# Performance work log

Hardware: AMD Instinct MI355X
Metric: run time of the kernel (lower is better)

Reference implementation:

```python
import jax, jax.numpy as jnp
import numpy as np

B, S, H, R, F, E, K = 4, 2048, 1024, 256, 4096, 8, 2


def setup_inputs() -> dict:
    key = jax.random.key(0)
    k = jax.random.split(key, 7)
    s = 0.02
    return {
        "x": jax.random.normal(k[0], (B, S, H), dtype=jnp.float32),
        "router_w": jax.random.normal(k[1], (H, E), dtype=jnp.float32) * s,
        "router_b": jnp.zeros((E,), dtype=jnp.float32),
        "w1": jax.random.normal(k[2], (E, H, R), dtype=jnp.float32) * s,  # expert Linear(hidden->rank), no bias
        "w2": jax.random.normal(k[3], (E, R, F), dtype=jnp.float32) * s,  # expert Linear(rank->ffn), no bias
        "lin2_w": jax.random.normal(k[4], (F, H), dtype=jnp.float32) * s,
        "lin2_b": jnp.zeros((H,), dtype=jnp.float32),
    }


def reference(x, router_w, router_b, w1, w2, lin2_w, lin2_b):
    # Router: softmax over experts, top-k selection (mask), weight by softmax prob
    logits = jnp.einsum("bsh,he->bse", x, router_w) + router_b
    routing_weights = jax.nn.softmax(logits, axis=-1)            # [B,S,E]
    _, topk_idx = jax.lax.top_k(routing_weights, K)              # [B,S,K]
    mask = jnp.sum(jax.nn.one_hot(topk_idx, E, dtype=x.dtype), axis=-2)  # [B,S,E] in {0,1}
    mw = routing_weights * mask                                  # mask * weight per expert

    # Dense per-expert low-rank FFN (original computes all experts, masks after).
    # Fold mask*weight into the rank-space activations to avoid a [B,S,E,F] tensor.
    t = jnp.einsum("bsh,ehr->bser", x, w1)                       # [B,S,E,R]
    t = t * mw[..., None]
    mixed = jnp.einsum("bser,erf->bsf", t, w2)                   # [B,S,F]

    h = jax.nn.gelu(mixed, approximate=False)                    # torch nn.GELU is erf-based
    out = jnp.einsum("bsf,fh->bsh", h, lin2_w) + lin2_b
    # dropout is identity in eval mode
    return out
```

## Files before the change

### kernel.cpp

```cpp
#include <hip/hip_runtime.h>
#include <math.h>


using short8  = __attribute__((ext_vector_type(8))) short;
using floatx4 = __attribute__((ext_vector_type(4))) float;
typedef unsigned short bf16_t;

#define TOK   8192
#define HDIM  1024
#define RDIM  256
#define FDIM  4096
#define NEXP  8
#define MAXTILES 96
#define MAXSLOTS 16384
#define IMG   16384

__device__ __forceinline__ bf16_t f2bf(float f) {
  union { float f; unsigned u; } a; a.f = f;
  unsigned u = a.u;
  return (bf16_t)((u + 0x7FFFu + ((u >> 16) & 1u)) >> 16);
}

__device__ __forceinline__ float gelu_erf(float v) {
  return 0.5f * v * (1.0f + erff(v * 0.70710678118654752f));
}

__device__ __forceinline__ void gload16(const void* g, void* l) {
  __builtin_amdgcn_global_load_lds(
      (const __attribute__((address_space(1))) void*)g,
      (__attribute__((address_space(3))) void*)l, 16, 0, 0);
}

__device__ __forceinline__ int swz_off(int r, int kl) {
  return r * 128 + ((((kl >> 3) ^ (r & 15)) << 3) | (kl & 7));
}


__device__ __forceinline__ void pack_tile_body(const float* __restrict__ src,
                                               size_t kStride,
                                               bf16_t* __restrict__ img,
                                               bf16_t* __restrict__ lim) {
  const int tid = threadIdx.x;
  const int rr = tid & 127, half = tid >> 7;
  for (int kl = half; kl < 128; kl += 2)
    lim[swz_off(rr, kl)] = f2bf(src[(size_t)kl * kStride + rr]);
  __syncthreads();
  const int4* s4 = (const int4*)lim;
  int4* d4 = (int4*)img;
#pragma unroll
  for (int i = 0; i < 8; i++) d4[tid + i * 256] = s4[tid + i * 256];
}

__global__ __launch_bounds__(256)
void prep(const float* __restrict__ x, const float* __restrict__ rw,
          const float* __restrict__ rb, const float* __restrict__ w1,
          const float* __restrict__ w2, const float* __restrict__ l2w,
          int* __restrict__ gid_tok, float2* __restrict__ tokscale,
          bf16_t* __restrict__ xb, bf16_t* __restrict__ w1p,
          bf16_t* __restrict__ w2p, bf16_t* __restrict__ ltw,
          int* __restrict__ tokslot, float2* __restrict__ slotsc) {
  __shared__ __align__(16) char smem[33280];
  const int b = blockIdx.x;
  const int t = threadIdx.x;

  if (b < 2048) {
    const int token = b * 4 + (t >> 6);
    const int lane  = t & 63;
    const float* xr = x + (size_t)token * HDIM;
    bf16_t* xbr = xb + (size_t)token * HDIM;
    double acc[NEXP];
#pragma unroll
    for (int e = 0; e < NEXP; e++) acc[e] = 0.0;
    for (int h = lane; h < HDIM; h += 64) {
      const float xf = xr[h];
      xbr[h] = f2bf(xf);
      const double xv = (double)xf;
      const float* wr = rw + (size_t)h * NEXP;
#pragma unroll
      for (int e = 0; e < NEXP; e++) acc[e] += xv * (double)wr[e];
    }
#pragma unroll
    for (int off = 32; off > 0; off >>= 1) {
#pragma unroll
      for (int e = 0; e < NEXP; e++) acc[e] += __shfl_xor(acc[e], off, 64);
    }
    double lg[NEXP];
#pragma unroll
    for (int e = 0; e < NEXP; e++) lg[e] = acc[e] + (double)rb[e];
    double mx = lg[0];
#pragma unroll
    for (int e = 1; e < NEXP; e++) mx = fmax(mx, lg[e]);
    double p[NEXP]; double den = 0.0;
#pragma unroll
    for (int e = 0; e < NEXP; e++) { p[e] = exp(lg[e] - mx); den += p[e]; }
    int i1 = 0;
#pragma unroll
    for (int e = 1; e < NEXP; e++) if (lg[e] > lg[i1]) i1 = e;
    int i2 = (i1 == 0) ? 1 : 0;
#pragma unroll
    for (int e = 0; e < NEXP; e++)
      if (e != i1 && e != i2 && lg[e] > lg[i2]) i2 = e;
    if (lane == 0) {
      const int elo = min(i1, i2), ehi = max(i1, i2);
      gid_tok[token] = elo * 8 + ehi;
      tokscale[token] = make_float2((float)(p[elo] / den), (float)(p[ehi] / den));
    }
  } else if (b < 2176) {
    const int img = b - 2048;
    const int e = img >> 4, nc = (img >> 3) & 1, kb = img & 7;
    pack_tile_body(w1 + (size_t)e * 1024 * 256 + (size_t)kb * 128 * 256 + nc * 128,
                   256, w1p + (size_t)img * IMG, (bf16_t*)smem);
  } else if (b < 2688) {
    const int img = b - 2176;
    const int n = img >> 4, e = (img >> 1) & 7, kb = img & 1;
    pack_tile_body(w2 + (size_t)e * 256 * 4096 + (size_t)kb * 128 * 4096 + n * 128,
                   4096, w2p + (size_t)img * IMG, (bf16_t*)smem);
  } else if (b < 3712) {
    float* tile = (float*)smem;
    const int bid = b - 2688;
    const int c0 = (bid & 15) * 64;
    const int r0 = (bid >> 4) * 64;
    const int tx = t & 63, ty = t >> 6;
#pragma unroll
    for (int i = 0; i < 64; i += 4)
      tile[(ty + i) * 65 + tx] = l2w[(size_t)(r0 + ty + i) * HDIM + (c0 + tx)];
    __syncthreads();
#pragma unroll
    for (int i = 0; i < 64; i += 4)
      ltw[(size_t)(c0 + ty + i) * FDIM + (r0 + tx)] = f2bf(tile[tx * 65 + ty + i]);
  } else {
    const int i = (b - 3712) * 256 + t;
    tokslot[i] = -1;
    slotsc[i] = make_float2(0.f, 0.f);
  }
}


__global__ void build_scatter(const int* __restrict__ gid_tok,
                              const float2* __restrict__ tokscale,
                              int* __restrict__ ctrl,
                              int* __restrict__ tok_of_slot,
                              float2* __restrict__ scale_of_slot) {
  __shared__ int hist[64], ntl[64], start[64], fill[64];
  const int t = threadIdx.x;
  if (t < 64) { hist[t] = 0; fill[t] = 0; }
  __syncthreads();
  for (int i = t; i < TOK; i += 256) atomicAdd(&hist[gid_tok[i]], 1);
  __syncthreads();
  if (t < 64) ntl[t] = (hist[t] + 127) >> 7;
  __syncthreads();
  if (t < 64) {
    int slot0 = 0, tile0 = 0;
    for (int g = 0; g < t; g++) { slot0 += ntl[g] << 7; tile0 += ntl[g]; }
    start[t] = slot0;
    const int nt = ntl[t], c = hist[t];
    for (int i = 0; i < nt; i++) {
      ctrl[256 + (tile0 + i) * 3 + 0] = t;
      ctrl[256 + (tile0 + i) * 3 + 1] = slot0 + i * 128;
      ctrl[256 + (tile0 + i) * 3 + 2] = min(128, c - i * 128);
    }
    if (t == 63) ctrl[192] = tile0 + nt;
  }
  __syncthreads();
  for (int i = t; i < TOK; i += 256) {
    const int g = gid_tok[i];
    const int pos = atomicAdd(&fill[g], 1);
    const int slot = start[g] + pos;
    tok_of_slot[slot] = i;
    scale_of_slot[slot] = tokscale[i];
  }
}

__global__ __launch_bounds__(256)
void gemm_g1(const bf16_t* __restrict__ xb, const bf16_t* __restrict__ w1p,
             bf16_t* __restrict__ Tp, const int* __restrict__ ctrl,
             const int* __restrict__ tok_of_slot,
             const float2* __restrict__ scale_of_slot) {
  const int b = blockIdx.x;
  const int n = b & 3, mh = (b >> 2) & 1, tile = b >> 3;
  if (tile >= ctrl[192]) return;
  const int nrows = ctrl[256 + tile * 3 + 2];
  if (mh && nrows <= 64) return;
  __shared__ bf16_t As[64 * 128];
  __shared__ bf16_t Bs[128 * 128];
  const int gid   = ctrl[256 + tile * 3];
  const int slot0 = ctrl[256 + tile * 3 + 1];
  const int e = (n < 2) ? (gid >> 3) : (gid & 7);
  const int nc = n & 1;
  const int tid = threadIdx.x, lane = tid & 63, w = tid >> 6;
  const int wm = (w & 1) * 32, wn = (w >> 1) * 64;
  const int l16 = lane & 15, quad = lane >> 4;

  floatx4 acc[2][4];
  const floatx4 zero = {0.f, 0.f, 0.f, 0.f};
#pragma unroll
  for (int i = 0; i < 2; i++)
#pragma unroll
    for (int j = 0; j < 4; j++) acc[i][j] = zero;

  int toks[4];
  int rowAs[4];
#pragma unroll
  for (int i = 0; i < 4; i++) {
    rowAs[i] = w * 16 + i * 4 + (lane >> 4);
    int tk = tok_of_slot[slot0 + mh * 64 + rowAs[i]];
    toks[i] = (tk < 0) ? 0 : tk;
  }
  const bf16_t* bimg = w1p + (size_t)(e * 16 + nc * 8) * IMG;
  bf16_t* lA = As + w * 2048;
  bf16_t* lB = Bs + w * 4096;

  for (int kb = 0; kb < 8; kb++) {
    __syncthreads();
#pragma unroll
    for (int i = 0; i < 4; i++) {
      const int gq = (lane & 15) ^ (rowAs[i] & 15);
      gload16(xb + (size_t)toks[i] * HDIM + kb * 128 + gq * 8, lA + i * 512);
    }
#pragma unroll
    for (int i = 0; i < 8; i++)
      gload16(bimg + (size_t)kb * IMG + w * 4096 + i * 512 + lane * 8, lB + i * 512);
    __syncthreads();
#pragma unroll
    for (int s = 0; s < 4; s++) {
      const int pg = ((s * 4 + quad) ^ l16) << 3;
      short8 af[2], bfr[4];
#pragma unroll
      for (int i = 0; i < 2; i++)
        af[i] = *(const short8*)&As[(wm + i * 16 + l16) * 128 + pg];
#pragma unroll
      for (int i = 0; i < 4; i++)
        bfr[i] = *(const short8*)&Bs[(wn + i * 16 + l16) * 128 + pg];
#pragma unroll
      for (int mi = 0; mi < 2; mi++)
#pragma unroll
        for (int ni = 0; ni < 4; ni++)
          acc[mi][ni] = __builtin_amdgcn_mfma_f32_16x16x32_bf16(
              af[mi], bfr[ni], acc[mi][ni], 0, 0, 0);
    }
  }

  __syncthreads();
#pragma unroll
  for (int mi = 0; mi < 2; mi++) {
#pragma unroll
    for (int r = 0; r < 4; r++) {
      const int rloc = wm + mi * 16 + quad * 4 + r;
      const float2 sc = scale_of_slot[slot0 + mh * 64 + rloc];
      const float s = (n < 2) ? sc.x : sc.y;
#pragma unroll
      for (int ni = 0; ni < 4; ni++) {
        const int c = wn + ni * 16 + l16;
        As[swz_off(rloc, c)] = f2bf(acc[mi][ni][r] * s);
      }
    }
  }
  __syncthreads();
  bf16_t* img = Tp + (size_t)(tile * 4 + n) * IMG + mh * 64 * 128;
  const int4* s4 = (const int4*)As;
  int4* d4 = (int4*)img;
#pragma unroll
  for (int j = 0; j < 4; j++) d4[tid + j * 256] = s4[tid + j * 256];
}

__global__ __launch_bounds__(256)
void gemm_g2(const bf16_t* __restrict__ Tp, const bf16_t* __restrict__ w2p,
             bf16_t* __restrict__ Hb, const int* __restrict__ ctrl,
             const int* __restrict__ tok_of_slot) {
  const int b = blockIdx.x;
  const int n = (b & 7) * 4 + ((b >> 3) & 3);
  const int mh = (b >> 5) & 1, tile = b >> 6;
  if (tile >= ctrl[192]) return;
  const int nrows = ctrl[256 + tile * 3 + 2];
  if (mh && nrows <= 64) return;
  __shared__ bf16_t As[64 * 128];
  __shared__ bf16_t Bs[128 * 128];
  const int gid   = ctrl[256 + tile * 3];
  const int slot0 = ctrl[256 + tile * 3 + 1];
  const int elo = gid >> 3, ehi = gid & 7;
  const int tid = threadIdx.x, lane = tid & 63, w = tid >> 6;
  const int wm = (w & 1) * 32, wn = (w >> 1) * 64;
  const int l16 = lane & 15, quad = lane >> 4;

  floatx4 acc[2][4];
  const floatx4 zero = {0.f, 0.f, 0.f, 0.f};
#pragma unroll
  for (int i = 0; i < 2; i++)
#pragma unroll
    for (int j = 0; j < 4; j++) acc[i][j] = zero;

  const bf16_t* aimg = Tp + (size_t)tile * 4 * IMG + mh * 64 * 128;
  bf16_t* lA = As + w * 2048;
  bf16_t* lB = Bs + w * 4096;

#pragma unroll
  for (int t = 0; t < 4; t++) {
    const int e = (t < 2) ? elo : ehi;
    const bf16_t* bimg = w2p + (size_t)(n * 16 + e * 2 + (t & 1)) * IMG;
    __syncthreads();
#pragma unroll
    for (int i = 0; i < 4; i++)
      gload16(aimg + (size_t)t * IMG + w * 2048 + i * 512 + lane * 8, lA + i * 512);
#pragma unroll
    for (int i = 0; i < 8; i++)
      gload16(bimg + w * 4096 + i * 512 + lane * 8, lB + i * 512);
    __syncthreads();
#pragma unroll
    for (int s = 0; s < 4; s++) {
      const int pg = ((s * 4 + quad) ^ l16) << 3;
      short8 af[2], bfr[4];
#pragma unroll
      for (int i = 0; i < 2; i++)
        af[i] = *(const short8*)&As[(wm + i * 16 + l16) * 128 + pg];
#pragma unroll
      for (int i = 0; i < 4; i++)
        bfr[i] = *(const short8*)&Bs[(wn + i * 16 + l16) * 128 + pg];
#pragma unroll
      for (int mi = 0; mi < 2; mi++)
#pragma unroll
        for (int ni = 0; ni < 4; ni++)
          acc[mi][ni] = __builtin_amdgcn_mfma_f32_16x16x32_bf16(
              af[mi], bfr[ni], acc[mi][ni], 0, 0, 0);
    }
  }

  __syncthreads();
#pragma unroll
  for (int mi = 0; mi < 2; mi++) {
#pragma unroll
    for (int r = 0; r < 4; r++) {
      const int rloc = wm + mi * 16 + quad * 4 + r;
#pragma unroll
      for (int ni = 0; ni < 4; ni++) {
        const int c = wn + ni * 16 + l16;
        Bs[rloc * 128 + c] = f2bf(gelu_erf(acc[mi][ni][r]));
      }
    }
  }
  __syncthreads();
  const int4* s4 = (const int4*)Bs;
#pragma unroll
  for (int j = 0; j < 4; j++) {
    const int chunk = tid + j * 256;
    const int row = chunk >> 4, off = chunk & 15;
    const int tok = tok_of_slot[slot0 + mh * 64 + row];
    if (tok >= 0)
      *(int4*)(Hb + (size_t)tok * FDIM + n * 128 + off * 8) = s4[chunk];
  }
}

__global__ __launch_bounds__(256)
void gemm_g3(const bf16_t* __restrict__ Hb, const bf16_t* __restrict__ ltw,
             float* __restrict__ out, float* __restrict__ p0) {
  __shared__ bf16_t As[128 * 64];
  __shared__ bf16_t Bs[128 * 64];
  const int b = blockIdx.x;
  const int r0 = b >> 3;
  const int m0 = ((b & 7) * 8 + (r0 & 7)) * 128;
  const int n0 = ((r0 >> 3) & 7) * 128;
  const int kb = r0 >> 6;
  const int tid = threadIdx.x, lane = tid & 63, w = tid >> 6;
  const int wm = (w >> 1) * 64, wn = (w & 1) * 64;
  const int l16 = lane & 15, quad = lane >> 4;
  const int rl = lane >> 3, gg = lane & 7;
  const int gf = (gg ^ rl) * 8;

  floatx4 acc[4][4];
  const floatx4 zero = {0.f, 0.f, 0.f, 0.f};
#pragma unroll
  for (int i = 0; i < 4; i++)
#pragma unroll
    for (int j = 0; j < 4; j++) acc[i][j] = zero;

  const bf16_t* ga[4];
  const bf16_t* gb[4];
#pragma unroll
  for (int c = 0; c < 4; c++) {
    ga[c] = Hb  + (size_t)(m0 + w * 32 + c * 8 + rl) * FDIM + kb * 2048 + gf;
    gb[c] = ltw + (size_t)(n0 + w * 32 + c * 8 + rl) * FDIM + kb * 2048 + gf;
  }
  bf16_t* lA = &As[w * 32 * 64];
  bf16_t* lB = &Bs[w * 32 * 64];

  for (int k0 = 0; k0 < 2048; k0 += 64) {
    __syncthreads();
#pragma unroll
    for (int c = 0; c < 4; c++) { gload16(ga[c], lA + c * 512); ga[c] += 64; }
#pragma unroll
    for (int c = 0; c < 4; c++) { gload16(gb[c], lB + c * 512); gb[c] += 64; }
    __syncthreads();
#pragma unroll
    for (int s = 0; s < 2; s++) {
      const int pg = ((s * 4 + quad) ^ (l16 & 7)) * 8;
      short8 af[4], bfr[4];
#pragma unroll
      for (int i = 0; i < 4; i++)
        af[i] = *(const short8*)&As[(wm + i * 16 + l16) * 64 + pg];
#pragma unroll
      for (int i = 0; i < 4; i++)
        bfr[i] = *(const short8*)&Bs[(wn + i * 16 + l16) * 64 + pg];
#pragma unroll
      for (int mi = 0; mi < 4; mi++)
#pragma unroll
        for (int ni = 0; ni < 4; ni++)
          acc[mi][ni] = __builtin_amdgcn_mfma_f32_16x16x32_bf16(
              af[mi], bfr[ni], acc[mi][ni], 0, 0, 0);
    }
  }

  float* dst = kb ? out : p0;
#pragma unroll
  for (int mi = 0; mi < 4; mi++) {
#pragma unroll
    for (int ni = 0; ni < 4; ni++) {
      const int row = m0 + wm + mi * 16 + quad * 4;
      const int col = n0 + wn + ni * 16 + l16;
#pragma unroll
      for (int r = 0; r < 4; r++)
        dst[(size_t)(row + r) * HDIM + col] = acc[mi][ni][r];
    }
  }
}

__global__ void reduce_out(float* __restrict__ out, const float* __restrict__ p0,
                           const float* __restrict__ bias) {
  const int i4 = blockIdx.x * 256 + threadIdx.x;
  float4 a = ((const float4*)out)[i4];
  float4 p = ((const float4*)p0)[i4];
  float4 bb = ((const float4*)bias)[i4 & 255];
  a.x += p.x + bb.x;
  a.y += p.y + bb.y;
  a.z += p.z + bb.z;
  a.w += p.w + bb.w;
  ((float4*)out)[i4] = a;
}


extern "C" void kernel_launch(void* const* d_in, const int* in_sizes, int n_in,
                              void* d_out, int out_size, void* d_ws, size_t ws_size,
                              hipStream_t stream) {
  const float* x   = (const float*)d_in[0];
  const float* rw  = (const float*)d_in[1];
  const float* rb  = (const float*)d_in[2];
  const float* w1  = (const float*)d_in[3];
  const float* w2  = (const float*)d_in[4];
  const float* l2w = (const float*)d_in[5];
  const float* l2b = (const float*)d_in[6];

  char* ws = (char*)d_ws;
  int*    ctrl     = (int*)   (ws + 0);
  int*    gid_tok  = (int*)   (ws + 4096);
  float2* tokscale = (float2*)(ws + 36864);
  int*    tokslot  = (int*)   (ws + 102400);
  float2* slotsc   = (float2*)(ws + 167936);
  bf16_t* xb  = (bf16_t*)(ws + 1048576);
  bf16_t* w1p = (bf16_t*)(ws + 17825792);
  bf16_t* w2p = (bf16_t*)(ws + 22020096);
  bf16_t* ltw = (bf16_t*)(ws + 38797312);
  bf16_t* Tp  = (bf16_t*)(ws + 47185920);
  bf16_t* Hb  = (bf16_t*)(ws + 59768832);
  float*  p0  = (float*) (ws + 1048576);

  prep<<<3776, 256, 0, stream>>>(x, rw, rb, w1, w2, l2w,
                                 gid_tok, tokscale, xb, w1p, w2p, ltw,
                                 tokslot, slotsc);
  build_scatter<<<1, 256, 0, stream>>>(gid_tok, tokscale, ctrl, tokslot, slotsc);

  gemm_g1<<<8 * MAXTILES, 256, 0, stream>>>(xb, w1p, Tp, ctrl, tokslot, slotsc);
  gemm_g2<<<64 * MAXTILES, 256, 0, stream>>>(Tp, w2p, Hb, ctrl, tokslot);
  gemm_g3<<<1024, 256, 0, stream>>>(Hb, ltw, (float*)d_out, p0);
  reduce_out<<<TOK * HDIM / 1024, 256, 0, stream>>>((float*)d_out, p0, l2b);
}
```

Before: 361.6 us.

## Fuse all stages into one cooperative persistent kernel with grid syncs

Replaces six separate launches with one cooperative kernel that runs the prep, build, scatter and three GEMM phases in grid-strided loops, separated by grid-wide barriers. The final GEMM no longer splits K in two, so the partial-sum buffer and the reduce kernel go away, and the bias is added in the epilogue. The scatter stage is spread across all blocks using global atomics instead of running in a single block. The aim is to remove launch gaps and the extra reduction pass, at the cost of grid-sync overhead, a capped persistent grid of at most 512 blocks that may hurt load balance, and fewer blocks in the last GEMM.

```diff
diff --git a/kernel.cpp b/kernel.cpp
--- a/kernel.cpp
+++ b/kernel.cpp
@@ -1,5 +1,8 @@
 #include <hip/hip_runtime.h>
+#include <hip/hip_cooperative_groups.h>
 #include <math.h>
+
+namespace cg = cooperative_groups;
 
 
 using short8  = __attribute__((ext_vector_type(8))) short;
@@ -12,8 +15,11 @@
 #define FDIM  4096
 #define NEXP  8
 #define MAXTILES 96
-#define MAXSLOTS 16384
 #define IMG   16384
+#define NPREP 3776
+#define NG1   (8 * MAXTILES)
+#define NG2   (64 * MAXTILES)
+#define NG3   512
 
 __device__ __forceinline__ bf16_t f2bf(float f) {
   union { float f; unsigned u; } a; a.f = f;
@@ -36,36 +42,19 @@
 }
 
 
-__device__ __forceinline__ void pack_tile_body(const float* __restrict__ src,
-                                               size_t kStride,
-                                               bf16_t* __restrict__ img,
-                                               bf16_t* __restrict__ lim) {
-  const int tid = threadIdx.x;
-  const int rr = tid & 127, half = tid >> 7;
-  for (int kl = half; kl < 128; kl += 2)
-    lim[swz_off(rr, kl)] = f2bf(src[(size_t)kl * kStride + rr]);
-  __syncthreads();
-  const int4* s4 = (const int4*)lim;
-  int4* d4 = (int4*)img;
-#pragma unroll
-  for (int i = 0; i < 8; i++) d4[tid + i * 256] = s4[tid + i * 256];
-}
-
-__global__ __launch_bounds__(256)
-void prep(const float* __restrict__ x, const float* __restrict__ rw,
-          const float* __restrict__ rb, const float* __restrict__ w1,
-          const float* __restrict__ w2, const float* __restrict__ l2w,
-          int* __restrict__ gid_tok, float2* __restrict__ tokscale,
-          bf16_t* __restrict__ xb, bf16_t* __restrict__ w1p,
-          bf16_t* __restrict__ w2p, bf16_t* __restrict__ ltw,
-          int* __restrict__ tokslot, float2* __restrict__ slotsc) {
-  __shared__ __align__(16) char smem[33280];
-  const int b = blockIdx.x;
+__device__ void phase_prep(int vb, char* smem,
+                           const float* __restrict__ x, const float* __restrict__ rw,
+                           const float* __restrict__ rb, const float* __restrict__ w1,
+                           const float* __restrict__ w2, const float* __restrict__ l2w,
+                           int* __restrict__ gid_tok, float2* __restrict__ tokscale,
+                           bf16_t* __restrict__ xb, bf16_t* __restrict__ w1p,
+                           bf16_t* __restrict__ w2p, bf16_t* __restrict__ ltw,
+                           int* __restrict__ tokslot, float2* __restrict__ slotsc,
+                           int* __restrict__ ctrl) {
   const int t = threadIdx.x;
-
-  if (b < 2048) {
-    const int token = b * 4 + (t >> 6);
-    const int lane  = t & 63;
+  const int lane = t & 63;
+  if (vb < 2048) {
+    const int token = vb * 4 + (t >> 6);
     const float* xr = x + (size_t)token * HDIM;
     bf16_t* xbr = xb + (size_t)token * HDIM;
     double acc[NEXP];
@@ -105,19 +94,31 @@
       gid_tok[token] = elo * 8 + ehi;
       tokscale[token] = make_float2((float)(p[elo] / den), (float)(p[ehi] / den));
     }
-  } else if (b < 2176) {
-    const int img = b - 2048;
-    const int e = img >> 4, nc = (img >> 3) & 1, kb = img & 7;
-    pack_tile_body(w1 + (size_t)e * 1024 * 256 + (size_t)kb * 128 * 256 + nc * 128,
-                   256, w1p + (size_t)img * IMG, (bf16_t*)smem);
-  } else if (b < 2688) {
-    const int img = b - 2176;
-    const int n = img >> 4, e = (img >> 1) & 7, kb = img & 1;
-    pack_tile_body(w2 + (size_t)e * 256 * 4096 + (size_t)kb * 128 * 4096 + n * 128,
-                   4096, w2p + (size_t)img * IMG, (bf16_t*)smem);
-  } else if (b < 3712) {
+  } else if (vb < 2688) {
+    const float* src; bf16_t* dst; size_t ks;
+    if (vb < 2176) {
+      const int img = vb - 2048;
+      const int e = img >> 4, nc = (img >> 3) & 1, kb = img & 7;
+      src = w1 + (size_t)e * 1024 * 256 + (size_t)kb * 128 * 256 + nc * 128;
+      ks = 256; dst = w1p + (size_t)img * IMG;
+    } else {
+      const int img = vb - 2176;
+      const int n = img >> 4, e = (img >> 1) & 7, kb = img & 1;
+      src = w2 + (size_t)e * 256 * 4096 + (size_t)kb * 128 * 4096 + n * 128;
+      ks = 4096; dst = w2p + (size_t)img * IMG;
+    }
+    bf16_t* lim = (bf16_t*)smem;
+    const int rr = t & 127, half = t >> 7;
+    for (int kl = half; kl < 128; kl += 2)
+      lim[swz_off(rr, kl)] = f2bf(src[(size_t)kl * ks + rr]);
+    __syncthreads();
+    const int4* s4 = (const int4*)lim;
+    int4* d4 = (int4*)dst;
+#pragma unroll
+    for (int i = 0; i < 8; i++) d4[t + i * 256] = s4[t + i * 256];
+  } else if (vb < 3712) {
     float* tile = (float*)smem;
-    const int bid = b - 2688;
+    const int bid = vb - 2688;
     const int c0 = (bid & 15) * 64;
     const int r0 = (bid >> 4) * 64;
     const int tx = t & 63, ty = t >> 6;
@@ -129,21 +130,19 @@
     for (int i = 0; i < 64; i += 4)
       ltw[(size_t)(c0 + ty + i) * FDIM + (r0 + tx)] = f2bf(tile[tx * 65 + ty + i]);
   } else {
-    const int i = (b - 3712) * 256 + t;
+    const int i = (vb - 3712) * 256 + t;
     tokslot[i] = -1;
     slotsc[i] = make_float2(0.f, 0.f);
-  }
-}
-
-
-__global__ void build_scatter(const int* __restrict__ gid_tok,
-                              const float2* __restrict__ tokscale,
-                              int* __restrict__ ctrl,
-                              int* __restrict__ tok_of_slot,
-                              float2* __restrict__ scale_of_slot) {
-  __shared__ int hist[64], ntl[64], start[64], fill[64];
+    if (vb == 3712 && t < 64) ctrl[64 + t] = 0;
+  }
+}
+
+__device__ void phase_build(char* smem, const int* __restrict__ gid_tok,
+                            int* __restrict__ ctrl) {
+  int* hist = (int*)smem;
+  int* ntl  = hist + 64;
   const int t = threadIdx.x;
-  if (t < 64) { hist[t] = 0; fill[t] = 0; }
+  if (t < 64) hist[t] = 0;
   __syncthreads();
   for (int i = t; i < TOK; i += 256) atomicAdd(&hist[gid_tok[i]], 1);
   __syncthreads();
@@ -152,7 +151,7 @@
   if (t < 64) {
     int slot0 = 0, tile0 = 0;
     for (int g = 0; g < t; g++) { slot0 += ntl[g] << 7; tile0 += ntl[g]; }
-    start[t] = slot0;
+    ctrl[128 + t] = slot0;
     const int nt = ntl[t], c = hist[t];
     for (int i = 0; i < nt; i++) {
       ctrl[256 + (tile0 + i) * 3 + 0] = t;
@@ -161,35 +160,39 @@
     }
     if (t == 63) ctrl[192] = tile0 + nt;
   }
-  __syncthreads();
-  for (int i = t; i < TOK; i += 256) {
+}
+
+__device__ void phase_scatter(int i0, int stride, const int* __restrict__ gid_tok,
+                              const float2* __restrict__ tokscale,
+                              int* __restrict__ ctrl, int* __restrict__ tokslot,
+                              float2* __restrict__ slotsc) {
+  for (int i = i0; i < TOK; i += stride) {
     const int g = gid_tok[i];
-    const int pos = atomicAdd(&fill[g], 1);
-    const int slot = start[g] + pos;
-    tok_of_slot[slot] = i;
-    scale_of_slot[slot] = tokscale[i];
-  }
-}
-
-__global__ __launch_bounds__(256)
-void gemm_g1(const bf16_t* __restrict__ xb, const bf16_t* __restrict__ w1p,
-             bf16_t* __restrict__ Tp, const int* __restrict__ ctrl,
-             const int* __restrict__ tok_of_slot,
-             const float2* __restrict__ scale_of_slot) {
-  const int b = blockIdx.x;
-  const int n = b & 3, mh = (b >> 2) & 1, tile = b >> 3;
+    const int pos = atomicAdd(&ctrl[64 + g], 1);
+    const int slot = ctrl[128 + g] + pos;
+    tokslot[slot] = i;
+    slotsc[slot] = tokscale[i];
+  }
+}
+
+__device__ void phase_g1(int vb, char* smem,
+                         const bf16_t* __restrict__ xb, const bf16_t* __restrict__ w1p,
+                         bf16_t* __restrict__ Tp, const int* __restrict__ ctrl,
+                         const int* __restrict__ tokslot,
+                         const float2* __restrict__ slotsc) {
+  const int n = vb & 3, mh = (vb >> 2) & 1, tile = vb >> 3;
   if (tile >= ctrl[192]) return;
   const int nrows = ctrl[256 + tile * 3 + 2];
   if (mh && nrows <= 64) return;
-  __shared__ bf16_t As[64 * 128];
-  __shared__ bf16_t Bs[128 * 128];
+  bf16_t* As = (bf16_t*)smem;
+  bf16_t* Bs = (bf16_t*)(smem + 16384);
   const int gid   = ctrl[256 + tile * 3];
   const int slot0 = ctrl[256 + tile * 3 + 1];
   const int e = (n < 2) ? (gid >> 3) : (gid & 7);
   const int nc = n & 1;
-  const int tid = threadIdx.x, lane = tid & 63, w = tid >> 6;
+  const int t = threadIdx.x, lane = t & 63, w = t >> 6;
+  const int l16 = lane & 15, quad = lane >> 4;
   const int wm = (w & 1) * 32, wn = (w >> 1) * 64;
-  const int l16 = lane & 15, quad = lane >> 4;
 
   floatx4 acc[2][4];
   const floatx4 zero = {0.f, 0.f, 0.f, 0.f};
@@ -198,12 +201,11 @@
 #pragma unroll
     for (int j = 0; j < 4; j++) acc[i][j] = zero;
 
-  int toks[4];
-  int rowAs[4];
+  int toks[4], rowAs[4];
 #pragma unroll
   for (int i = 0; i < 4; i++) {
     rowAs[i] = w * 16 + i * 4 + (lane >> 4);
-    int tk = tok_of_slot[slot0 + mh * 64 + rowAs[i]];
+    int tk = tokslot[slot0 + mh * 64 + rowAs[i]];
     toks[i] = (tk < 0) ? 0 : tk;
   }
   const bf16_t* bimg = w1p + (size_t)(e * 16 + nc * 8) * IMG;
@@ -246,7 +248,7 @@
 #pragma unroll
     for (int r = 0; r < 4; r++) {
       const int rloc = wm + mi * 16 + quad * 4 + r;
-      const float2 sc = scale_of_slot[slot0 + mh * 64 + rloc];
+      const float2 sc = slotsc[slot0 + mh * 64 + rloc];
       const float s = (n < 2) ? sc.x : sc.y;
 #pragma unroll
       for (int ni = 0; ni < 4; ni++) {
@@ -260,27 +262,26 @@
   const int4* s4 = (const int4*)As;
   int4* d4 = (int4*)img;
 #pragma unroll
-  for (int j = 0; j < 4; j++) d4[tid + j * 256] = s4[tid + j * 256];
-}
-
-__global__ __launch_bounds__(256)
-void gemm_g2(const bf16_t* __restrict__ Tp, const bf16_t* __restrict__ w2p,
-             bf16_t* __restrict__ Hb, const int* __restrict__ ctrl,
-             const int* __restrict__ tok_of_slot) {
-  const int b = blockIdx.x;
-  const int n = (b & 7) * 4 + ((b >> 3) & 3);
-  const int mh = (b >> 5) & 1, tile = b >> 6;
+  for (int j = 0; j < 4; j++) d4[t + j * 256] = s4[t + j * 256];
+}
+
+__device__ void phase_g2(int vb, char* smem,
+                         const bf16_t* __restrict__ Tp, const bf16_t* __restrict__ w2p,
+                         bf16_t* __restrict__ Hb, const int* __restrict__ ctrl,
+                         const int* __restrict__ tokslot) {
+  const int n = (vb & 7) * 4 + ((vb >> 3) & 3);
+  const int mh = (vb >> 5) & 1, tile = vb >> 6;
   if (tile >= ctrl[192]) return;
   const int nrows = ctrl[256 + tile * 3 + 2];
   if (mh && nrows <= 64) return;
-  __shared__ bf16_t As[64 * 128];
-  __shared__ bf16_t Bs[128 * 128];
+  bf16_t* As = (bf16_t*)smem;
+  bf16_t* Bs = (bf16_t*)(smem + 16384);
   const int gid   = ctrl[256 + tile * 3];
   const int slot0 = ctrl[256 + tile * 3 + 1];
   const int elo = gid >> 3, ehi = gid & 7;
-  const int tid = threadIdx.x, lane = tid & 63, w = tid >> 6;
+  const int t = threadIdx.x, lane = t & 63, w = t >> 6;
+  const int l16 = lane & 15, quad = lane >> 4;
   const int wm = (w & 1) * 32, wn = (w >> 1) * 64;
-  const int l16 = lane & 15, quad = lane >> 4;
 
   floatx4 acc[2][4];
   const floatx4 zero = {0.f, 0.f, 0.f, 0.f};
@@ -294,13 +295,13 @@
   bf16_t* lB = Bs + w * 4096;
 
 #pragma unroll
-  for (int t = 0; t < 4; t++) {
-    const int e = (t < 2) ? elo : ehi;
-    const bf16_t* bimg = w2p + (size_t)(n * 16 + e * 2 + (t & 1)) * IMG;
+  for (int tt = 0; tt < 4; tt++) {
+    const int e = (tt < 2) ? elo : ehi;
+    const bf16_t* bimg = w2p + (size_t)(n * 16 + e * 2 + (tt & 1)) * IMG;
     __syncthreads();
 #pragma unroll
     for (int i = 0; i < 4; i++)
-      gload16(aimg + (size_t)t * IMG + w * 2048 + i * 512 + lane * 8, lA + i * 512);
+      gload16(aimg + (size_t)tt * IMG + w * 2048 + i * 512 + lane * 8, lA + i * 512);
 #pragma unroll
     for (int i = 0; i < 8; i++)
       gload16(bimg + w * 4096 + i * 512 + lane * 8, lB + i * 512);
@@ -341,29 +342,26 @@
   const int4* s4 = (const int4*)Bs;
 #pragma unroll
   for (int j = 0; j < 4; j++) {
-    const int chunk = tid + j * 256;
+    const int chunk = t + j * 256;
     const int row = chunk >> 4, off = chunk & 15;
-    const int tok = tok_of_slot[slot0 + mh * 64 + row];
+    const int tok = tokslot[slot0 + mh * 64 + row];
     if (tok >= 0)
       *(int4*)(Hb + (size_t)tok * FDIM + n * 128 + off * 8) = s4[chunk];
   }
 }
 
-__global__ __launch_bounds__(256)
-void gemm_g3(const bf16_t* __restrict__ Hb, const bf16_t* __restrict__ ltw,
-             float* __restrict__ out, float* __restrict__ p0) {
-  __shared__ bf16_t As[128 * 64];
-  __shared__ bf16_t Bs[128 * 64];
-  const int b = blockIdx.x;
-  const int r0 = b >> 3;
-  const int m0 = ((b & 7) * 8 + (r0 & 7)) * 128;
-  const int n0 = ((r0 >> 3) & 7) * 128;
-  const int kb = r0 >> 6;
-  const int tid = threadIdx.x, lane = tid & 63, w = tid >> 6;
+__device__ void phase_g3(int vb, char* smem,
+                         const bf16_t* __restrict__ Hb, const bf16_t* __restrict__ ltw,
+                         float* __restrict__ out, const float* __restrict__ bias) {
+  bf16_t* As = (bf16_t*)smem;
+  bf16_t* Bs = (bf16_t*)(smem + 16384);
+  const int m0 = ((vb & 7) * 8 + ((vb >> 3) & 7)) * 128;
+  const int n0 = (vb >> 6) * 128;
+  const int t = threadIdx.x, lane = t & 63, w = t >> 6;
+  const int l16 = lane & 15, quad = lane >> 4;
   const int wm = (w >> 1) * 64, wn = (w & 1) * 64;
-  const int l16 = lane & 15, quad = lane >> 4;
-  const int rl = lane >> 3, gg = lane & 7;
-  const int gf = (gg ^ rl) * 8;
+  const int rl = lane >> 3, gq = lane & 7;
+  const int gf = (gq ^ rl) * 8;
 
   floatx4 acc[4][4];
   const floatx4 zero = {0.f, 0.f, 0.f, 0.f};
@@ -376,13 +374,13 @@
   const bf16_t* gb[4];
 #pragma unroll
   for (int c = 0; c < 4; c++) {
-    ga[c] = Hb  + (size_t)(m0 + w * 32 + c * 8 + rl) * FDIM + kb * 2048 + gf;
-    gb[c] = ltw + (size_t)(n0 + w * 32 + c * 8 + rl) * FDIM + kb * 2048 + gf;
-  }
-  bf16_t* lA = &As[w * 32 * 64];
-  bf16_t* lB = &Bs[w * 32 * 64];
-
-  for (int k0 = 0; k0 < 2048; k0 += 64) {
+    ga[c] = Hb  + (size_t)(m0 + w * 32 + c * 8 + rl) * FDIM + gf;
+    gb[c] = ltw + (size_t)(n0 + w * 32 + c * 8 + rl) * FDIM + gf;
+  }
+  bf16_t* lA = As + w * 2048;
+  bf16_t* lB = Bs + w * 2048;
+
+  for (int k0 = 0; k0 < FDIM; k0 += 64) {
     __syncthreads();
 #pragma unroll
     for (int c = 0; c < 4; c++) { gload16(ga[c], lA + c * 512); ga[c] += 64; }
@@ -408,7 +406,6 @@
     }
   }
 
-  float* dst = kb ? out : p0;
 #pragma unroll
   for (int mi = 0; mi < 4; mi++) {
 #pragma unroll
@@ -417,22 +414,81 @@
       const int col = n0 + wn + ni * 16 + l16;
 #pragma unroll
       for (int r = 0; r < 4; r++)
-        dst[(size_t)(row + r) * HDIM + col] = acc[mi][ni][r];
-    }
-  }
-}
-
-__global__ void reduce_out(float* __restrict__ out, const float* __restrict__ p0,
-                           const float* __restrict__ bias) {
-  const int i4 = blockIdx.x * 256 + threadIdx.x;
-  float4 a = ((const float4*)out)[i4];
-  float4 p = ((const float4*)p0)[i4];
-  float4 bb = ((const float4*)bias)[i4 & 255];
-  a.x += p.x + bb.x;
-  a.y += p.y + bb.y;
-  a.z += p.z + bb.z;
-  a.w += p.w + bb.w;
-  ((float4*)out)[i4] = a;
+        out[(size_t)(row + r) * HDIM + col] = acc[mi][ni][r] + bias[col];
+    }
+  }
+}
+
+
+__global__ __launch_bounds__(256, 2)
+void mega(const float* x, const float* rw, const float* rb, const float* w1,
+          const float* w2, const float* l2w, const float* l2b,
+          int* gid_tok, float2* tokscale, bf16_t* xb, bf16_t* w1p,
+          bf16_t* w2p, bf16_t* ltw, int* tokslot, float2* slotsc,
+          int* ctrl, bf16_t* Tp, bf16_t* Hb, float* out) {
+  cg::grid_group gg = cg::this_grid();
+  __shared__ __align__(16) char smem[49152];
+  const int b = blockIdx.x, G = gridDim.x;
+  for (int vb = b; vb < NPREP; vb += G) {
+    __syncthreads();
+    phase_prep(vb, smem, x, rw, rb, w1, w2, l2w, gid_tok, tokscale,
+               xb, w1p, w2p, ltw, tokslot, slotsc, ctrl);
+  }
+  gg.sync();
+  if (b == 0) phase_build(smem, gid_tok, ctrl);
+  gg.sync();
+  phase_scatter(b * 256 + threadIdx.x, G * 256, gid_tok, tokscale, ctrl,
+                tokslot, slotsc);
+  gg.sync();
+  for (int vb = b; vb < NG1; vb += G)
+    phase_g1(vb, smem, xb, w1p, Tp, ctrl, tokslot, slotsc);
+  gg.sync();
+  for (int vb = b; vb < NG2; vb += G)
+    phase_g2(vb, smem, Tp, w2p, Hb, ctrl, tokslot);
+  gg.sync();
+  for (int vb = b; vb < NG3; vb += G)
+    phase_g3(vb, smem, Hb, ltw, out, l2b);
+}
+
+__global__ __launch_bounds__(256)
+void k_prep(const float* x, const float* rw, const float* rb, const float* w1,
+            const float* w2, const float* l2w, int* gid_tok, float2* tokscale,
+            bf16_t* xb, bf16_t* w1p, bf16_t* w2p, bf16_t* ltw,
+            int* tokslot, float2* slotsc, int* ctrl) {
+  __shared__ __align__(16) char smem[32768];
+  phase_prep(blockIdx.x, smem, x, rw, rb, w1, w2, l2w, gid_tok, tokscale,
+             xb, w1p, w2p, ltw, tokslot, slotsc, ctrl);
+}
+
+__global__ void k_build(const int* gid_tok, int* ctrl) {
+  __shared__ __align__(16) char smem[512];
+  phase_build(smem, gid_tok, ctrl);
+}
+
+__global__ void k_scatter(const int* gid_tok, const float2* tokscale, int* ctrl,
+                          int* tokslot, float2* slotsc) {
+  phase_scatter(blockIdx.x * 256 + threadIdx.x, gridDim.x * 256, gid_tok,
+                tokscale, ctrl, tokslot, slotsc);
+}
+
+__global__ __launch_bounds__(256)
+void k_g1(const bf16_t* xb, const bf16_t* w1p, bf16_t* Tp, const int* ctrl,
+          const int* tokslot, const float2* slotsc) {
+  __shared__ __align__(16) char smem[49152];
+  phase_g1(blockIdx.x, smem, xb, w1p, Tp, ctrl, tokslot, slotsc);
+}
+
+__global__ __launch_bounds__(256)
+void k_g2(const bf16_t* Tp, const bf16_t* w2p, bf16_t* Hb, const int* ctrl,
+          const int* tokslot) {
+  __shared__ __align__(16) char smem[49152];
+  phase_g2(blockIdx.x, smem, Tp, w2p, Hb, ctrl, tokslot);
+}
+
+__global__ __launch_bounds__(256)
+void k_g3(const bf16_t* Hb, const bf16_t* ltw, float* out, const float* bias) {
+  __shared__ __align__(16) char smem[32768];
+  phase_g3(blockIdx.x, smem, Hb, ltw, out, bias);
 }
 
 
@@ -459,15 +515,35 @@
   bf16_t* ltw = (bf16_t*)(ws + 38797312);
   bf16_t* Tp  = (bf16_t*)(ws + 47185920);
   bf16_t* Hb  = (bf16_t*)(ws + 59768832);
-  float*  p0  = (float*) (ws + 1048576);
-
-  prep<<<3776, 256, 0, stream>>>(x, rw, rb, w1, w2, l2w,
-                                 gid_tok, tokscale, xb, w1p, w2p, ltw,
-                                 tokslot, slotsc);
-  build_scatter<<<1, 256, 0, stream>>>(gid_tok, tokscale, ctrl, tokslot, slotsc);
-
-  gemm_g1<<<8 * MAXTILES, 256, 0, stream>>>(xb, w1p, Tp, ctrl, tokslot, slotsc);
-  gemm_g2<<<64 * MAXTILES, 256, 0, stream>>>(Tp, w2p, Hb, ctrl, tokslot);
-  gemm_g3<<<1024, 256, 0, stream>>>(Hb, ltw, (float*)d_out, p0);
-  reduce_out<<<TOK * HDIM / 1024, 256, 0, stream>>>((float*)d_out, p0, l2b);
-}
+  float*  outp = (float*)d_out;
+
+  int nb = 0;
+  hipError_t err = hipOccupancyMaxActiveBlocksPerMultiprocessor(
+      &nb, (const void*)mega, 256, 0);
+  if (err == hipSuccess && nb > 0) {
+    int grid = nb * 256;
+    if (grid > 512) grid = 512;
+    void* args[] = {
+      (void*)&x, (void*)&rw, (void*)&rb, (void*)&w1, (void*)&w2, (void*)&l2w,
+      (void*)&l2b, (void*)&gid_tok, (void*)&tokscale, (void*)&xb, (void*)&w1p,
+      (void*)&w2p, (void*)&ltw, (void*)&tokslot, (void*)&slotsc, (void*)&ctrl,
+      (void*)&Tp, (void*)&Hb, (void*)&outp,
+    };
+    err = hipLaunchCooperativeKernel((const void*)mega, dim3(grid), dim3(256),
+                                     args, 0, stream);
+  } else if (err == hipSuccess) {
+    err = hipErrorUnknown;
+  }
+
+  if (err != hipSuccess) {
+    k_prep<<<NPREP, 256, 0, stream>>>(x, rw, rb, w1, w2, l2w, gid_tok,
+                                      tokscale, xb, w1p, w2p, ltw,
+                                      tokslot, slotsc, ctrl);
+    k_build<<<1, 256, 0, stream>>>(gid_tok, ctrl);
+    k_scatter<<<TOK / 256 / 8, 256, 0, stream>>>(gid_tok, tokscale, ctrl,
+                                                 tokslot, slotsc);
+    k_g1<<<NG1, 256, 0, stream>>>(xb, w1p, Tp, ctrl, tokslot, slotsc);
+    k_g2<<<NG2, 256, 0, stream>>>(Tp, w2p, Hb, ctrl, tokslot);
+    k_g3<<<NG3, 256, 0, stream>>>(Hb, ltw, outp, l2b);
+  }
+}
```

Result: slower. 773.1 us (+113.8%).
